# Performance work log

Hardware: AMD Instinct MI355X
Metric: run time of the kernel (lower is better)

Reference implementation:

```python
import jax, jax.numpy as jnp
import numpy as np
from jax import lax


def setup_inputs() -> dict:
    key = jax.random.key(0)
    ks = jax.random.split(key, 8)
    B, H, W = 1, 128, 128

    def rnd(k, shape, fan_in):
        return jax.random.normal(k, shape, dtype=jnp.float32) / np.float32(np.sqrt(fan_in))

    return {
        "x": jax.random.normal(ks[0], (B, 1, H, W), dtype=jnp.float32),
        "z": jax.random.uniform(ks[1], (B, 1), dtype=jnp.float32),
        "w_conv1": rnd(ks[2], (16, 1, 9, 9), 81),
        "b_conv1": jnp.zeros((16,), jnp.float32),
        "w_conv2": rnd(ks[3], (16, 16, 5, 5), 16 * 25),
        "b_conv2": jnp.zeros((16,), jnp.float32),
        "w_fc1": rnd(ks[4], (1024, 128), 1024),
        "b_fc1": jnp.zeros((128,), jnp.float32),
        "w_pose": rnd(ks[5], (1, 16), 1),
        "b_pose": jnp.zeros((16,), jnp.float32),
        "w_fc2": rnd(ks[6], (144, 1), 144),
        "b_fc2": jnp.zeros((1,), jnp.float32),
    }


_DN = ("NCHW", "OIHW", "NCHW")  # conv dimension numbers
_P = 32  # GQ-CNN patch size


def _maxpool2(h):
    return lax.reduce_window(h, -jnp.inf, lax.max, (1, 1, 2, 2), (1, 1, 2, 2), "VALID")


def _gqcnn(patches, z_rep, w_conv1, b_conv1, w_conv2, b_conv2,
           w_fc1, b_fc1, w_pose, b_pose, w_fc2, b_fc2):
    # patches: [N,1,32,32], z_rep: [N,1] -> quality [N,1]
    h = jax.nn.relu(lax.conv_general_dilated(patches, w_conv1, (1, 1), "SAME",
                                             dimension_numbers=_DN)
                    + b_conv1[None, :, None, None])
    h = _maxpool2(h)  # [N,16,16,16]
    h = jax.nn.relu(lax.conv_general_dilated(h, w_conv2, (1, 1), "SAME",
                                             dimension_numbers=_DN)
                    + b_conv2[None, :, None, None])
    h = _maxpool2(h)  # [N,16,8,8]
    flat = h.reshape(h.shape[0], -1)  # [N,1024]
    f = jax.nn.relu(flat @ w_fc1 + b_fc1)      # [N,128]
    p = jax.nn.relu(z_rep @ w_pose + b_pose)   # [N,16]
    return jnp.concatenate([f, p], axis=1) @ w_fc2 + b_fc2  # [N,1]


def reference(x, z, w_conv1, b_conv1, w_conv2, b_conv2,
              w_fc1, b_fc1, w_pose, b_pose, w_fc2, b_fc2):
    B, _, H, W = x.shape
    Hp, Wp = H - _P, W - _P  # loop ranges in the original: range(H-32), range(W-32)
    # Batched patch extraction replaces the O(H*W) Python loop.
    pat = lax.conv_general_dilated_patches(x, (_P, _P), (1, 1), "VALID")  # [B,1024,H-31,W-31]
    pat = pat[:, :, :Hp, :Wp]
    pat = jnp.transpose(pat, (0, 2, 3, 1)).reshape(B * Hp * Wp, 1, _P, _P)
    z_rep = jnp.repeat(z, Hp * Wp, axis=0)  # matches [B,Hp,Wp] flattening order
    q = _gqcnn(pat, z_rep, w_conv1, b_conv1, w_conv2, b_conv2,
               w_fc1, b_fc1, w_pose, b_pose, w_fc2, b_fc2)  # [N,1]
    half = _P // 2
    heat = jnp.zeros_like(x).at[:, :, half:H - half, half:W - half].set(
        q.reshape(B, 1, Hp, Wp))
    return heat
```

## Files before the change

### kernel.cpp

```cpp
#include <hip/hip_runtime.h>

typedef __attribute__((ext_vector_type(8))) short short8;
typedef __attribute__((ext_vector_type(4))) float f32x4;
typedef unsigned short u16;

__device__ __forceinline__ u16 f2bf(float f) {
    unsigned u = __builtin_bit_cast(unsigned, f);
    unsigned r = u + 0x7fffu + ((u >> 16) & 1u);
    return (u16)(r >> 16);
}
__device__ __forceinline__ unsigned pkbf(float lo, float hi) {
    unsigned r;
    asm("v_cvt_pk_bf16_f32 %0, %1, %2" : "=v"(r) : "v"(lo), "v"(hi));
    return r;
}

__global__ __launch_bounds__(256) void k0_prep(
    const float* __restrict__ z, const float* __restrict__ w1,
    const float* __restrict__ w2, const float* __restrict__ wfc1,
    const float* __restrict__ wpose, const float* __restrict__ bpose,
    const float* __restrict__ wfc2, const float* __restrict__ bfc2,
    float* __restrict__ out, u16* __restrict__ w1p, u16* __restrict__ w2p,
    u16* __restrict__ fc1T)
{
    int gt = blockIdx.x * 256 + threadIdx.x;

    {
        float zz = z[0];
        float s = bfc2[0];
        #pragma unroll
        for (int j = 0; j < 16; ++j) {
            float p = fmaxf(zz * wpose[j] + bpose[j], 0.f);
            s += p * wfc2[128 + j];
        }
        int y = gt >> 7, x = gt & 127;
        bool interior = (y >= 16) && (y < 112) && (x >= 16) && (x < 112);
        out[gt] = interior ? s : 0.f;
    }

    if (gt < 2560) {
        int l = (gt >> 3) & 63, j = gt & 7, s = gt >> 9;
        int o = l & 15, bq = l >> 4;
        u16 v = 0;
        if (bq < 3) {
            int dx = bq * 4 + (j & 3);
            int dy = -1;
            if (s < 4) dy = 2 * s + (j >> 2);
            else if (j < 4) dy = 8;
            if (dy >= 0 && dx <= 8) v = f2bf(w1[o * 81 + dy * 9 + dx]);
        }
        w1p[gt] = v;
    }
    if (gt < 6656) {
        int l = (gt >> 3) & 63, j = gt & 7, s = gt >> 9;
        int o = l & 15, bq = l >> 4;
        int dy, dx, c8; bool valid = true;
        if (s < 5)       { dy = s;     dx = bq >> 1;       c8 = bq & 1; }
        else if (s < 10) { dy = s - 5; dx = 2 + (bq >> 1); c8 = bq & 1; }
        else { dy = (s - 10) + 3 * (bq & 1); dx = 4; c8 = bq >> 1; valid = (dy <= 4); }
        int ci = c8 * 8 + j;
        w2p[gt] = valid ? f2bf(w2[o * 400 + ci * 25 + dy * 5 + dx]) : (u16)0;
    }
    {
        int base = gt * 8;
        int n = base >> 10, kk = base & 1023;
        short8 v;
        #pragma unroll
        for (int j = 0; j < 8; ++j) v[j] = (short)f2bf(wfc1[(kk + j) * 128 + n]);
        *(short8*)&fc1T[base] = v;
    }
}

__global__ __launch_bounds__(256, 2) void k1_feat(
    const float* __restrict__ x, const u16* __restrict__ w1p,
    const u16* __restrict__ w2p, const float* __restrict__ b1g,
    const float* __restrict__ b2g, u16* __restrict__ feat)
{
    __shared__ unsigned s2[40 * 44];
    __shared__ u16 s_h1p[20 * 20 * 24];
    __shared__ unsigned s_feat[512];

    const int tid = threadIdx.x;
    const int lane = tid & 63;
    const int wv = tid >> 6;
    const int mm = lane & 15;
    const int bq = lane >> 4;
    const int blk = blockIdx.x;
    const int py = blk / 96, px = blk % 96;

    {
        uint4 z4 = {0, 0, 0, 0};
        for (int i = tid; i < 152; i += 256) {
            int dst;
            if (i < 88) { int r8 = i / 11, c4 = i % 11;
                          int row = (r8 < 4) ? r8 : 32 + r8; dst = row * 11 + c4; }
            else        { int j = i - 88; dst = (4 + (j >> 1)) * 11 + 9 + (j & 1); }
            ((uint4*)s2)[dst] = z4;
        }
        for (int i = tid; i < 1200; i += 256) ((uint4*)s_h1p)[i] = z4;
    }

    short8 w1f[5], w2f[13];
    #pragma unroll
    for (int s = 0; s < 5; ++s) w1f[s] = *(const short8*)&w1p[(s * 64 + lane) * 8];
    #pragma unroll
    for (int s = 0; s < 13; ++s) w2f[s] = *(const short8*)&w2p[(s * 64 + lane) * 8];
    const float bias1 = b1g[mm], bias2 = b2g[mm];

    for (int task = tid; task < 288; task += 256) {
        int ir = task / 9, g = task - ir * 9;
        int ic0 = g * 4 - 4;
        const float* xr = x + (py + ir) * 128 + px;
        float v[5];
        #pragma unroll
        for (int vi = 0; vi < 5; ++vi) {
            int ic = ic0 + vi;
            v[vi] = (ic >= 0 && ic < 32) ? xr[ic] : 0.f;
        }
        uint4 w;
        w.x = pkbf(v[0], v[1]);
        w.y = pkbf(v[1], v[2]);
        w.z = pkbf(v[2], v[3]);
        w.w = pkbf(v[3], v[4]);
        *(uint4*)&s2[(4 + ir) * 44 + g * 4] = w;
    }
    __syncthreads();

    union F { short8 s; unsigned u[4]; };
    const int dxq = (bq == 3) ? 0 : bq;

    for (int qi = 0; qi < 4; ++qi) {
        int q = wv + qi * 4;
        const unsigned* pb0 = &s2[(2 * q) * 44 + mm + dxq * 4];
        const unsigned* pb1 = pb0 + 16;
        f32x4 ac0 = {0, 0, 0, 0}, ac1 = {0, 0, 0, 0};
        f32x4 ac2 = {0, 0, 0, 0}, ac3 = {0, 0, 0, 0};
        #pragma unroll
        for (int s = 0; s < 5; ++s) {
            const int ra  = 2 * s * 44;
            const int blo = (s < 4) ? (2 * s + 1) * 44 : 9 * 44;
            const int bhi = (s < 4) ? (2 * s + 2) * 44 : 8 * 44;
            F fa0, fa1, fb0, fb1;
            fa0.u[0] = pb0[ra];      fa0.u[1] = pb0[ra + 2];
            fa0.u[2] = pb0[ra + 44]; fa0.u[3] = pb0[ra + 46];
            fa1.u[0] = pb1[ra];      fa1.u[1] = pb1[ra + 2];
            fa1.u[2] = pb1[ra + 44]; fa1.u[3] = pb1[ra + 46];
            fb0.u[0] = pb0[blo];     fb0.u[1] = pb0[blo + 2];
            fb0.u[2] = pb0[bhi];     fb0.u[3] = pb0[bhi + 2];
            fb1.u[0] = pb1[blo];     fb1.u[1] = pb1[blo + 2];
            fb1.u[2] = pb1[bhi];     fb1.u[3] = pb1[bhi + 2];
            ac0 = __builtin_amdgcn_mfma_f32_16x16x32_bf16(fa0.s, w1f[s], ac0, 0, 0, 0);
            ac2 = __builtin_amdgcn_mfma_f32_16x16x32_bf16(fa1.s, w1f[s], ac2, 0, 0, 0);
            ac1 = __builtin_amdgcn_mfma_f32_16x16x32_bf16(fb0.s, w1f[s], ac1, 0, 0, 0);
            ac3 = __builtin_amdgcn_mfma_f32_16x16x32_bf16(fb1.s, w1f[s], ac3, 0, 0, 0);
        }
        #pragma unroll
        for (int h = 0; h < 2; ++h) {
            f32x4 aA = h ? ac2 : ac0, aB = h ? ac3 : ac1;
            float vr0, vr1;
            {
                float a0 = fmaxf(fmaxf(aA[0], aA[1]), fmaxf(aB[0], aB[1]));
                vr0 = fmaxf(a0 + bias1, 0.f);
                float a1 = fmaxf(fmaxf(aA[2], aA[3]), fmaxf(aB[2], aB[3]));
                vr1 = fmaxf(a1 + bias1, 0.f);
            }
            unsigned pw = pkbf(vr0, vr1);
            int pc = h * 8 + (bq << 1);
            int cb = ((2 + q) * 20 + (2 + pc)) * 24 + mm;
            s_h1p[cb] = (u16)pw;
            s_h1p[cb + 24] = (u16)(pw >> 16);
        }
    }
    __syncthreads();

    {
        const int q0 = wv, q1 = wv + 4;
        const int c8s = (bq & 1) * 8;
        const int baseA0 = ((2 * q0) * 20 + mm + (bq >> 1)) * 24 + c8s;
        const int baseA1 = ((2 * q1) * 20 + mm + (bq >> 1)) * 24 + c8s;
        const int baseB0 = baseA0 + 2 * 24;
        const int baseB1 = baseA1 + 2 * 24;
        const int c8C = (bq >> 1) * 8;
        const int yC0 = 2 * q0 + 3 * (bq & 1);
        const int yC1 = 2 * q1 + 3 * (bq & 1);
        f32x4 p0A = {0, 0, 0, 0}, p0B = {0, 0, 0, 0};
        f32x4 p1A = {0, 0, 0, 0}, p1B = {0, 0, 0, 0};

        short8 a0 = *(const short8*)&s_h1p[baseA0];
        short8 a1 = *(const short8*)&s_h1p[baseA1];
        #pragma unroll
        for (int s = 0; s < 5; ++s) {
            short8 n0 = *(const short8*)&s_h1p[baseA0 + (s + 1) * 480];
            short8 n1 = *(const short8*)&s_h1p[baseA1 + (s + 1) * 480];
            p0A = __builtin_amdgcn_mfma_f32_16x16x32_bf16(a0, w2f[s], p0A, 0, 0, 0);
            p1A = __builtin_amdgcn_mfma_f32_16x16x32_bf16(a1, w2f[s], p1A, 0, 0, 0);
            p0B = __builtin_amdgcn_mfma_f32_16x16x32_bf16(n0, w2f[s], p0B, 0, 0, 0);
            p1B = __builtin_amdgcn_mfma_f32_16x16x32_bf16(n1, w2f[s], p1B, 0, 0, 0);
            a0 = n0; a1 = n1;
        }
        a0 = *(const short8*)&s_h1p[baseB0];
        a1 = *(const short8*)&s_h1p[baseB1];
        #pragma unroll
        for (int s = 0; s < 5; ++s) {
            short8 n0 = *(const short8*)&s_h1p[baseB0 + (s + 1) * 480];
            short8 n1 = *(const short8*)&s_h1p[baseB1 + (s + 1) * 480];
            p0A = __builtin_amdgcn_mfma_f32_16x16x32_bf16(a0, w2f[5 + s], p0A, 0, 0, 0);
            p1A = __builtin_amdgcn_mfma_f32_16x16x32_bf16(a1, w2f[5 + s], p1A, 0, 0, 0);
            p0B = __builtin_amdgcn_mfma_f32_16x16x32_bf16(n0, w2f[5 + s], p0B, 0, 0, 0);
            p1B = __builtin_amdgcn_mfma_f32_16x16x32_bf16(n1, w2f[5 + s], p1B, 0, 0, 0);
            a0 = n0; a1 = n1;
        }
        {
            int y00 = yC0, y10 = (yC1 > 19) ? 19 : yC1;
            a0 = *(const short8*)&s_h1p[(y00 * 20 + mm + 4) * 24 + c8C];
            a1 = *(const short8*)&s_h1p[(y10 * 20 + mm + 4) * 24 + c8C];
        }
        #pragma unroll
        for (int s = 0; s < 3; ++s) {
            int y0n = yC0 + s + 1; if (y0n > 19) y0n = 19;
            int y1n = yC1 + s + 1; if (y1n > 19) y1n = 19;
            short8 n0 = *(const short8*)&s_h1p[(y0n * 20 + mm + 4) * 24 + c8C];
            short8 n1 = *(const short8*)&s_h1p[(y1n * 20 + mm + 4) * 24 + c8C];
            p0A = __builtin_amdgcn_mfma_f32_16x16x32_bf16(a0, w2f[10 + s], p0A, 0, 0, 0);
            p1A = __builtin_amdgcn_mfma_f32_16x16x32_bf16(a1, w2f[10 + s], p1A, 0, 0, 0);
            p0B = __builtin_amdgcn_mfma_f32_16x16x32_bf16(n0, w2f[10 + s], p0B, 0, 0, 0);
            p1B = __builtin_amdgcn_mfma_f32_16x16x32_bf16(n1, w2f[10 + s], p1B, 0, 0, 0);
            a0 = n0; a1 = n1;
        }
        #pragma unroll
        for (int pi = 0; pi < 2; ++pi) {
            f32x4 aA = pi ? p1A : p0A, aB = pi ? p1B : p0B;
            int q = pi ? q1 : q0;
            float v0, v1;
            {
                float a = fmaxf(fmaxf(aA[0], aA[1]), fmaxf(aB[0], aB[1]));
                v0 = fmaxf(a + bias2, 0.f);
                float b = fmaxf(fmaxf(aA[2], aA[3]), fmaxf(aB[2], aB[3]));
                v1 = fmaxf(b + bias2, 0.f);
            }
            unsigned dwv = pkbf(v0, v1);
            s_feat[mm * 32 + ((q * 4 + bq) ^ mm)] = dwv;
        }
    }
    __syncthreads();

    {
        int ci = tid >> 4, t = tid & 15;
        uint2 v;
        v.x = s_feat[ci * 32 + ((2 * t) ^ ci)];
        v.y = s_feat[ci * 32 + ((2 * t + 1) ^ ci)];
        *(uint2*)&feat[blk * 1024 + tid * 4] = v;
    }
}

__global__ __launch_bounds__(256) void k2_fc(
    const u16* __restrict__ feat, const u16* __restrict__ fc1T,
    const float* __restrict__ bfc1, const float* __restrict__ wfc2,
    float* __restrict__ out)
{
    __shared__ u16 sA[64 * 136];
    __shared__ u16 sB[32 * 136];
    const int tid = threadIdx.x;
    const int lane = tid & 63;
    const int wv = tid >> 6;
    const int mm = lane & 15;
    const int bq = lane >> 4;
    const int p0 = (blockIdx.x % 144) * 64;
    const int n0 = (blockIdx.x / 144) * 32;

    f32x4 acc[2];
    acc[0] = (f32x4){0, 0, 0, 0};
    acc[1] = (f32x4){0, 0, 0, 0};

    for (int kt = 0; kt < 8; ++kt) {
        for (int i = tid; i < 1024; i += 256) {
            int row = i >> 4, ch = i & 15;
            *(short8*)&sA[row * 136 + ch * 8] =
                *(const short8*)&feat[(p0 + row) * 1024 + kt * 128 + ch * 8];
        }
        for (int i = tid; i < 512; i += 256) {
            int row = i >> 4, ch = i & 15;
            *(short8*)&sB[row * 136 + ch * 8] =
                *(const short8*)&fc1T[(n0 + row) * 1024 + kt * 128 + ch * 8];
        }
        __syncthreads();
        #pragma unroll
        for (int ks = 0; ks < 4; ++ks) {
            short8 aF = *(const short8*)&sA[(wv * 16 + mm) * 136 + ks * 32 + bq * 8];
            #pragma unroll
            for (int nt = 0; nt < 2; ++nt) {
                short8 bF = *(const short8*)&sB[(nt * 16 + mm) * 136 + ks * 32 + bq * 8];
                acc[nt] = __builtin_amdgcn_mfma_f32_16x16x32_bf16(aF, bF, acc[nt], 0, 0, 0);
            }
        }
        __syncthreads();
    }

    float qs[4] = {0, 0, 0, 0};
    #pragma unroll
    for (int nt = 0; nt < 2; ++nt) {
        int n = n0 + nt * 16 + mm;
        float bb = bfc1[n], wf = wfc2[n];
        #pragma unroll
        for (int r = 0; r < 4; ++r) {
            float f = fmaxf(acc[nt][r] + bb, 0.f);
            qs[r] += f * wf;
        }
    }
    #pragma unroll
    for (int r = 0; r < 4; ++r) {
        float v = qs[r];
        v += __shfl_xor(v, 1);
        v += __shfl_xor(v, 2);
        v += __shfl_xor(v, 4);
        v += __shfl_xor(v, 8);
        qs[r] = v;
    }
    if (mm == 0) {
        #pragma unroll
        for (int r = 0; r < 4; ++r) {
            int p = p0 + wv * 16 + bq * 4 + r;
            int qy = p / 96, qx = p % 96;
            atomicAdd(&out[(16 + qy) * 128 + (16 + qx)], qs[r]);
        }
    }
}

extern "C" void kernel_launch(void* const* d_in, const int* in_sizes, int n_in,
                              void* d_out, int out_size, void* d_ws, size_t ws_size,
                              hipStream_t stream)
{
    const float* x     = (const float*)d_in[0];
    const float* z     = (const float*)d_in[1];
    const float* w1    = (const float*)d_in[2];
    const float* b1    = (const float*)d_in[3];
    const float* w2    = (const float*)d_in[4];
    const float* b2    = (const float*)d_in[5];
    const float* wfc1  = (const float*)d_in[6];
    const float* bfc1  = (const float*)d_in[7];
    const float* wpose = (const float*)d_in[8];
    const float* bpose = (const float*)d_in[9];
    const float* wfc2  = (const float*)d_in[10];
    const float* bfc2  = (const float*)d_in[11];
    float* out = (float*)d_out;

    char* ws = (char*)d_ws;
    u16*   w1p  = (u16*)(ws + 0);
    u16*   w2p  = (u16*)(ws + 8192);
    u16*   fc1T = (u16*)(ws + 24576);
    u16*   feat = (u16*)(ws + 294912);

    hipLaunchKernelGGL(k0_prep, dim3(64), dim3(256), 0, stream,
                       z, w1, w2, wfc1, wpose, bpose, wfc2, bfc2,
                       out, w1p, w2p, fc1T);
    hipLaunchKernelGGL(k1_feat, dim3(9216), dim3(256), 0, stream,
                       x, w1p, w2p, b1, b2, feat);
    hipLaunchKernelGGL(k2_fc, dim3(576), dim3(256), 0, stream,
                       feat, fc1T, bfc1, wfc2, out);
}
```

Before: 99.84 us.

## Swizzle conv1 LDS layout, widen FC tile, and stage fc1 transpose through LDS

Three changes. The conv1 output buffer in shared memory gets an XOR swizzle on the 8-channel slot, keyed on spatial position, to cut bank conflicts in the conv2 MFMA operand reads. The FC kernel tile grows from 32 to 64 output columns, halving the grid and the number of times the feature matrix is reloaded, at the cost of fewer blocks and more LDS per block. The fc1 weight transpose in the prep kernel now stages through LDS, so the strided global reads become coalesced.

```diff
diff --git a/kernel.cpp b/kernel.cpp
--- a/kernel.cpp
+++ b/kernel.cpp
@@ -14,6 +14,8 @@
     asm("v_cvt_pk_bf16_f32 %0, %1, %2" : "=v"(r) : "v"(lo), "v"(hi));
     return r;
 }
+
+#define SW(yx, sl) ((yx) * 24 + ((((sl) ^ (((yx) >> 3) & 1))) << 3))
 
 __global__ __launch_bounds__(256) void k0_prep(
     const float* __restrict__ z, const float* __restrict__ w1,
@@ -23,7 +25,9 @@
     float* __restrict__ out, u16* __restrict__ w1p, u16* __restrict__ w2p,
     u16* __restrict__ fc1T)
 {
-    int gt = blockIdx.x * 256 + threadIdx.x;
+    __shared__ float ldsf[2048];
+    int tid = threadIdx.x;
+    int gt = blockIdx.x * 256 + tid;
 
     {
         float zz = z[0];
@@ -61,13 +65,19 @@
         int ci = c8 * 8 + j;
         w2p[gt] = valid ? f2bf(w2[o * 400 + ci * 25 + dy * 5 + dx]) : (u16)0;
     }
-    {
-        int base = gt * 8;
-        int n = base >> 10, kk = base & 1023;
+
+    {
+        int kt0 = blockIdx.x * 16;
+        for (int i = tid; i < 2048; i += 256) {
+            int ki = i >> 7, n = i & 127;
+            ldsf[i] = wfc1[(kt0 + ki) * 128 + n];
+        }
+        __syncthreads();
+        int n = tid >> 1, kh = (tid & 1) * 8;
         short8 v;
         #pragma unroll
-        for (int j = 0; j < 8; ++j) v[j] = (short)f2bf(wfc1[(kk + j) * 128 + n]);
-        *(short8*)&fc1T[base] = v;
+        for (int j = 0; j < 8; ++j) v[j] = (short)f2bf(ldsf[(kh + j) * 128 + n]);
+        *(short8*)&fc1T[n * 1024 + kt0 + kh] = v;
     }
 }
 
@@ -166,44 +176,42 @@
             }
             unsigned pw = pkbf(vr0, vr1);
             int pc = h * 8 + (bq << 1);
-            int cb = ((2 + q) * 20 + (2 + pc)) * 24 + mm;
-            s_h1p[cb] = (u16)pw;
-            s_h1p[cb + 24] = (u16)(pw >> 16);
+            int yx0 = (2 + q) * 20 + 2 + pc;
+            int yx1 = yx0 + 1;
+            s_h1p[yx0 * 24 + (mm ^ ((((yx0) >> 3) & 1) << 3))] = (u16)pw;
+            s_h1p[yx1 * 24 + (mm ^ ((((yx1) >> 3) & 1) << 3))] = (u16)(pw >> 16);
         }
     }
     __syncthreads();
 
     {
-        const int q0 = wv, q1 = wv + 4;
-        const int c8s = (bq & 1) * 8;
-        const int baseA0 = ((2 * q0) * 20 + mm + (bq >> 1)) * 24 + c8s;
-        const int baseA1 = ((2 * q1) * 20 + mm + (bq >> 1)) * 24 + c8s;
-        const int baseB0 = baseA0 + 2 * 24;
-        const int baseB1 = baseA1 + 2 * 24;
-        const int c8C = (bq >> 1) * 8;
-        const int yC0 = 2 * q0 + 3 * (bq & 1);
-        const int yC1 = 2 * q1 + 3 * (bq & 1);
+        const int slotAB = bq & 1;
+        const int yxA0 = 40 * wv + mm + (bq >> 1);
+        const int yxA1 = yxA0 + 160;
+        const int slotC = bq >> 1;
+        const int yC0 = 2 * wv + 3 * (bq & 1);
+        const int yC1 = yC0 + 8;
         f32x4 p0A = {0, 0, 0, 0}, p0B = {0, 0, 0, 0};
         f32x4 p1A = {0, 0, 0, 0}, p1B = {0, 0, 0, 0};
 
-        short8 a0 = *(const short8*)&s_h1p[baseA0];
-        short8 a1 = *(const short8*)&s_h1p[baseA1];
+        short8 a0 = *(const short8*)&s_h1p[SW(yxA0, slotAB)];
+        short8 a1 = *(const short8*)&s_h1p[SW(yxA1, slotAB)];
         #pragma unroll
         for (int s = 0; s < 5; ++s) {
-            short8 n0 = *(const short8*)&s_h1p[baseA0 + (s + 1) * 480];
-            short8 n1 = *(const short8*)&s_h1p[baseA1 + (s + 1) * 480];
+            short8 n0 = *(const short8*)&s_h1p[SW(yxA0 + 20 * (s + 1), slotAB)];
+            short8 n1 = *(const short8*)&s_h1p[SW(yxA1 + 20 * (s + 1), slotAB)];
             p0A = __builtin_amdgcn_mfma_f32_16x16x32_bf16(a0, w2f[s], p0A, 0, 0, 0);
             p1A = __builtin_amdgcn_mfma_f32_16x16x32_bf16(a1, w2f[s], p1A, 0, 0, 0);
             p0B = __builtin_amdgcn_mfma_f32_16x16x32_bf16(n0, w2f[s], p0B, 0, 0, 0);
             p1B = __builtin_amdgcn_mfma_f32_16x16x32_bf16(n1, w2f[s], p1B, 0, 0, 0);
             a0 = n0; a1 = n1;
         }
-        a0 = *(const short8*)&s_h1p[baseB0];
-        a1 = *(const short8*)&s_h1p[baseB1];
+        a0 = *(const short8*)&s_h1p[SW(yxA0 + 2, slotAB)];
+        a1 = *(const short8*)&s_h1p[SW(yxA1 + 2, slotAB)];
         #pragma unroll
         for (int s = 0; s < 5; ++s) {
-            short8 n0 = *(const short8*)&s_h1p[baseB0 + (s + 1) * 480];
-            short8 n1 = *(const short8*)&s_h1p[baseB1 + (s + 1) * 480];
+            short8 n0 = *(const short8*)&s_h1p[SW(yxA0 + 2 + 20 * (s + 1), slotAB)];
+            short8 n1 = *(const short8*)&s_h1p[SW(yxA1 + 2 + 20 * (s + 1), slotAB)];
             p0A = __builtin_amdgcn_mfma_f32_16x16x32_bf16(a0, w2f[5 + s], p0A, 0, 0, 0);
             p1A = __builtin_amdgcn_mfma_f32_16x16x32_bf16(a1, w2f[5 + s], p1A, 0, 0, 0);
             p0B = __builtin_amdgcn_mfma_f32_16x16x32_bf16(n0, w2f[5 + s], p0B, 0, 0, 0);
@@ -212,15 +220,15 @@
         }
         {
             int y00 = yC0, y10 = (yC1 > 19) ? 19 : yC1;
-            a0 = *(const short8*)&s_h1p[(y00 * 20 + mm + 4) * 24 + c8C];
-            a1 = *(const short8*)&s_h1p[(y10 * 20 + mm + 4) * 24 + c8C];
+            a0 = *(const short8*)&s_h1p[SW(y00 * 20 + mm + 4, slotC)];
+            a1 = *(const short8*)&s_h1p[SW(y10 * 20 + mm + 4, slotC)];
         }
         #pragma unroll
         for (int s = 0; s < 3; ++s) {
             int y0n = yC0 + s + 1; if (y0n > 19) y0n = 19;
             int y1n = yC1 + s + 1; if (y1n > 19) y1n = 19;
-            short8 n0 = *(const short8*)&s_h1p[(y0n * 20 + mm + 4) * 24 + c8C];
-            short8 n1 = *(const short8*)&s_h1p[(y1n * 20 + mm + 4) * 24 + c8C];
+            short8 n0 = *(const short8*)&s_h1p[SW(y0n * 20 + mm + 4, slotC)];
+            short8 n1 = *(const short8*)&s_h1p[SW(y1n * 20 + mm + 4, slotC)];
             p0A = __builtin_amdgcn_mfma_f32_16x16x32_bf16(a0, w2f[10 + s], p0A, 0, 0, 0);
             p1A = __builtin_amdgcn_mfma_f32_16x16x32_bf16(a1, w2f[10 + s], p1A, 0, 0, 0);
             p0B = __builtin_amdgcn_mfma_f32_16x16x32_bf16(n0, w2f[10 + s], p0B, 0, 0, 0);
@@ -230,7 +238,7 @@
         #pragma unroll
         for (int pi = 0; pi < 2; ++pi) {
             f32x4 aA = pi ? p1A : p0A, aB = pi ? p1B : p0B;
-            int q = pi ? q1 : q0;
+            int q = pi ? (wv + 4) : wv;
             float v0, v1;
             {
                 float a = fmaxf(fmaxf(aA[0], aA[1]), fmaxf(aB[0], aB[1]));
@@ -259,18 +267,18 @@
     float* __restrict__ out)
 {
     __shared__ u16 sA[64 * 136];
-    __shared__ u16 sB[32 * 136];
+    __shared__ u16 sB[64 * 136];
     const int tid = threadIdx.x;
     const int lane = tid & 63;
     const int wv = tid >> 6;
     const int mm = lane & 15;
     const int bq = lane >> 4;
     const int p0 = (blockIdx.x % 144) * 64;
-    const int n0 = (blockIdx.x / 144) * 32;
-
-    f32x4 acc[2];
-    acc[0] = (f32x4){0, 0, 0, 0};
-    acc[1] = (f32x4){0, 0, 0, 0};
+    const int n0 = (blockIdx.x / 144) * 64;
+
+    f32x4 acc[4];
+    #pragma unroll
+    for (int i = 0; i < 4; ++i) acc[i] = (f32x4){0, 0, 0, 0};
 
     for (int kt = 0; kt < 8; ++kt) {
         for (int i = tid; i < 1024; i += 256) {
@@ -278,7 +286,7 @@
             *(short8*)&sA[row * 136 + ch * 8] =
                 *(const short8*)&feat[(p0 + row) * 1024 + kt * 128 + ch * 8];
         }
-        for (int i = tid; i < 512; i += 256) {
+        for (int i = tid; i < 1024; i += 256) {
             int row = i >> 4, ch = i & 15;
             *(short8*)&sB[row * 136 + ch * 8] =
                 *(const short8*)&fc1T[(n0 + row) * 1024 + kt * 128 + ch * 8];
@@ -288,7 +296,7 @@
         for (int ks = 0; ks < 4; ++ks) {
             short8 aF = *(const short8*)&sA[(wv * 16 + mm) * 136 + ks * 32 + bq * 8];
             #pragma unroll
-            for (int nt = 0; nt < 2; ++nt) {
+            for (int nt = 0; nt < 4; ++nt) {
                 short8 bF = *(const short8*)&sB[(nt * 16 + mm) * 136 + ks * 32 + bq * 8];
                 acc[nt] = __builtin_amdgcn_mfma_f32_16x16x32_bf16(aF, bF, acc[nt], 0, 0, 0);
             }
@@ -298,7 +306,7 @@
 
     float qs[4] = {0, 0, 0, 0};
     #pragma unroll
-    for (int nt = 0; nt < 2; ++nt) {
+    for (int nt = 0; nt < 4; ++nt) {
         int n = n0 + nt * 16 + mm;
         float bb = bfc1[n], wf = wfc2[n];
         #pragma unroll
@@ -355,6 +363,6 @@
                        out, w1p, w2p, fc1T);
     hipLaunchKernelGGL(k1_feat, dim3(9216), dim3(256), 0, stream,
                        x, w1p, w2p, b1, b2, feat);
-    hipLaunchKernelGGL(k2_fc, dim3(576), dim3(256), 0, stream,
+    hipLaunchKernelGGL(k2_fc, dim3(288), dim3(256), 0, stream,
                        feat, fc1T, bfc1, wfc2, out);
 }
```

Result: slower. 106.0 us (+6.2%).
